# Optimization experiments

Measured on AMD Instinct MI355X. Metric: run time of the kernel, lower is better.

## Reference

```python
import jax, jax.numpy as jnp
import numpy as np

SINKHORN_ITERS = 100
SINKHORN_EPS = 0.1


def setup_inputs() -> dict:
    key = jax.random.key(0)
    k1, k2 = jax.random.split(key)
    M, N, C = 2048, 2048, 512
    d_M_q = jax.random.normal(k1, (M, C), dtype=jnp.float32)
    d_N_r = jax.random.normal(k2, (N, C), dtype=jnp.float32)
    # pipeline feeds L2-normalized descriptors (F.normalize(..., p=2, dim=1))
    d_M_q = d_M_q / jnp.linalg.norm(d_M_q, axis=1, keepdims=True)
    d_N_r = d_N_r / jnp.linalg.norm(d_N_r, axis=1, keepdims=True)
    z = jnp.float32(0.5)  # learned bin_score scalar
    return {"d_M_q": d_M_q, "d_N_r": d_N_r, "z": z}


def reference(d_M_q, d_N_r, z):
    M, N = d_M_q.shape[0], d_N_r.shape[0]
    # score matmul: (M, C) x (C, N) -> (M, N)
    score = jnp.einsum('mc,nc->mn', d_M_q, d_N_r)
    # augmented (M+1, N+1): dustbin row/col/corner filled with z
    S_aug = jnp.full((M + 1, N + 1), z, dtype=d_M_q.dtype).at[:M, :N].set(score)
    K0 = jnp.exp(S_aug / SINKHORN_EPS)

    def body(i, K):
        K = K / K.sum(axis=1, keepdims=True)  # row normalize
        K = K / K.sum(axis=0, keepdims=True)  # col normalize
        return K

    P_aug = jax.lax.fori_loop(0, SINKHORN_ITERS, body, K0)
    P = P_aug[:M, :N]
    return P, P_aug
```

## Files before the change

### kernel.cpp

```cpp
#include <hip/hip_runtime.h>
#include <hip/hip_fp16.h>

#define ITERS 100
#define AGENT __HIP_MEMORY_SCOPE_AGENT

union PK { unsigned long long u; struct { float v; unsigned tag; } s; };

#define SLOT 136
#define MSG_ONE (2 * 16 * 16 * SLOT)
#define UV_STRIDE 272

__device__ __forceinline__ float wave_sum(float p) {
    p += __shfl_xor(p, 1, 64);
    p += __shfl_xor(p, 2, 64);
    p += __shfl_xor(p, 4, 64);
    p += __shfl_xor(p, 8, 64);
    p += __shfl_xor(p, 16, 64);
    p += __shfl_xor(p, 32, 64);
    return p;
}

__global__ void __launch_bounds__(256, 1)
sinkhorn_fused(const float* __restrict__ Q, const float* __restrict__ R,
               const float* __restrict__ zp, float* __restrict__ out,
               unsigned long long* __restrict__ ws)
{
    __shared__ __align__(16) char smem[65536];
    float* As = (float*)smem;
    float* Bs = (float*)(smem + 32768);
    char*  TrmB = smem;
    char*  TcmB = smem + 32768;

    const int t  = threadIdx.x;
    const int b  = blockIdx.x;
    const int bi = b >> 4, bj = b & 15;
    const int tx = t & 15, ty = t >> 4;
    const int l  = t & 63, w  = t >> 6;
    const int gi0 = bi * 128, gj0 = bj * 128;

    float acc[8][8];
#pragma unroll
    for (int r = 0; r < 8; r++)
#pragma unroll
        for (int c = 0; c < 8; c++) acc[r][c] = 0.f;

    const int lr = t & 31, lc4 = t >> 5;
    const float* Qb = Q + (size_t)gi0 * 512;
    const float* Rb = R + (size_t)gj0 * 512;

    float4 qa[4], ra[4];
#pragma unroll
    for (int i = 0; i < 4; i++) {
        qa[i] = *(const float4*)(Qb + (size_t)(lr + 32 * i) * 512 + 4 * lc4);
        ra[i] = *(const float4*)(Rb + (size_t)(lr + 32 * i) * 512 + 4 * lc4);
    }
#pragma unroll
    for (int i = 0; i < 4; i++) {
        int row = lr + 32 * i;
        As[(4*lc4+0)*128 + row] = qa[i].x;  As[(4*lc4+1)*128 + row] = qa[i].y;
        As[(4*lc4+2)*128 + row] = qa[i].z;  As[(4*lc4+3)*128 + row] = qa[i].w;
        Bs[(4*lc4+0)*128 + row] = ra[i].x;  Bs[(4*lc4+1)*128 + row] = ra[i].y;
        Bs[(4*lc4+2)*128 + row] = ra[i].z;  Bs[(4*lc4+3)*128 + row] = ra[i].w;
    }
    __syncthreads();

    for (int ks = 0; ks < 16; ks++) {
        if (ks < 15) {
            int k0 = (ks + 1) * 32;
#pragma unroll
            for (int i = 0; i < 4; i++) {
                qa[i] = *(const float4*)(Qb + (size_t)(lr+32*i)*512 + k0 + 4*lc4);
                ra[i] = *(const float4*)(Rb + (size_t)(lr+32*i)*512 + k0 + 4*lc4);
            }
        }
        const float* A = As + (ks & 1) * (32 * 128);
        const float* B = Bs + (ks & 1) * (32 * 128);
#pragma unroll 4
        for (int k = 0; k < 32; k++) {
            float4 a0 = *(const float4*)(A + k*128 + 8*ty);
            float4 a1 = *(const float4*)(A + k*128 + 8*ty + 4);
            float4 b0 = *(const float4*)(B + k*128 + 8*tx);
            float4 b1 = *(const float4*)(B + k*128 + 8*tx + 4);
            float av[8] = {a0.x,a0.y,a0.z,a0.w,a1.x,a1.y,a1.z,a1.w};
            float bv[8] = {b0.x,b0.y,b0.z,b0.w,b1.x,b1.y,b1.z,b1.w};
#pragma unroll
            for (int r = 0; r < 8; r++)
#pragma unroll
                for (int c = 0; c < 8; c++)
                    acc[r][c] = fmaf(av[r], bv[c], acc[r][c]);
        }
        if (ks < 15) {
            __syncthreads();
            float* An = As + ((ks+1) & 1) * (32 * 128);
            float* Bn = Bs + ((ks+1) & 1) * (32 * 128);
#pragma unroll
            for (int i = 0; i < 4; i++) {
                int row = lr + 32 * i;
                An[(4*lc4+0)*128 + row] = qa[i].x;  An[(4*lc4+1)*128 + row] = qa[i].y;
                An[(4*lc4+2)*128 + row] = qa[i].z;  An[(4*lc4+3)*128 + row] = qa[i].w;
                Bn[(4*lc4+0)*128 + row] = ra[i].x;  Bn[(4*lc4+1)*128 + row] = ra[i].y;
                Bn[(4*lc4+2)*128 + row] = ra[i].z;  Bn[(4*lc4+3)*128 + row] = ra[i].w;
            }
            __syncthreads();
        }
    }
    __syncthreads();

    const float E = expf(zp[0] * 10.0f);
#pragma unroll
    for (int r = 0; r < 8; r++)
#pragma unroll
        for (int c = 0; c < 8; c++) acc[r][c] = expf(acc[r][c] * 10.0f);

#pragma unroll
    for (int r = 0; r < 8; r++) {
        int rr = 8 * ty + r;
        unsigned short h[8];
#pragma unroll
        for (int c = 0; c < 8; c++) h[c] = __half_as_ushort(__float2half(acc[r][c]));
        uint4 pk;
        pk.x = h[0] | ((unsigned)h[1] << 16); pk.y = h[2] | ((unsigned)h[3] << 16);
        pk.z = h[4] | ((unsigned)h[5] << 16); pk.w = h[6] | ((unsigned)h[7] << 16);
        *(uint4*)(TrmB + rr * 256 + ((tx ^ (rr & 15)) << 4)) = pk;
    }
#pragma unroll
    for (int c = 0; c < 8; c++) {
        int cc = 8 * tx + c;
        unsigned short h[8];
#pragma unroll
        for (int r = 0; r < 8; r++) h[r] = __half_as_ushort(__float2half(acc[r][c]));
        uint4 pk;
        pk.x = h[0] | ((unsigned)h[1] << 16); pk.y = h[2] | ((unsigned)h[3] << 16);
        pk.z = h[4] | ((unsigned)h[5] << 16); pk.w = h[6] | ((unsigned)h[7] << 16);
        *(uint4*)(TcmB + cc * 256 + ((ty ^ (cc & 15)) << 4)) = pk;
    }

    unsigned long long* rmsg = ws;
    unsigned long long* cmsg = ws + MSG_ONE;
    float* uvb  = (float*)(ws + 2 * MSG_ONE) + b * UV_STRIDE;
    float* ubuf = uvb;
    float* vbuf = uvb + 136;

    if (t < 128)      vbuf[t] = 1.0f;
    else if (t < 130) vbuf[t] = 64.0f;
    float uN = 0.f, vN = 1.0f, vsum = 128.0f, usum = 0.f;
    __syncthreads();

    for (int it = 0; it < ITERS; it++) {
        const int buf = it & 1;
        const unsigned tagw = (unsigned)(it + 1);

        {
            unsigned long long* base = rmsg + (size_t)((buf * 16 + bi) * 16) * SLOT;
            if (t == 128) {
                PK p; p.s.v = vsum; p.s.tag = tagw;
                __hip_atomic_store(base + (size_t)bj * SLOT + 128, p.u, __ATOMIC_RELAXED, AGENT);
            }
            if (t < 128) {
                const char* rp = TrmB + t * 256;
                const float4* v4 = (const float4*)vbuf;
                float racc = 0.f;
#pragma unroll
                for (int c = 0; c < 16; c++) {
                    uint4 kq = *(const uint4*)(rp + ((c ^ (t & 15)) << 4));
                    float4 va = v4[2 * c], vb = v4[2 * c + 1];
                    const __half2* h2 = (const __half2*)&kq;
                    float2 f;
                    f = __half22float2(h2[0]); racc = fmaf(f.x, va.x, fmaf(f.y, va.y, racc));
                    f = __half22float2(h2[1]); racc = fmaf(f.x, va.z, fmaf(f.y, va.w, racc));
                    f = __half22float2(h2[2]); racc = fmaf(f.x, vb.x, fmaf(f.y, vb.y, racc));
                    f = __half22float2(h2[3]); racc = fmaf(f.x, vb.z, fmaf(f.y, vb.w, racc));
                }
                PK p; p.s.v = racc; p.s.tag = tagw;
                __hip_atomic_store(base + (size_t)bj * SLOT + t, p.u, __ATOMIC_RELAXED, AGENT);
            }
            if (t < 128) {
                bool vdone = (l >= 16);
                float vsv = 0.f, rsum = 0.f;
                for (;;) {
                    PK m[16];
#pragma unroll
                    for (int s = 0; s < 16; s++)
                        m[s].u = __hip_atomic_load(base + (size_t)s * SLOT + t,
                                                   __ATOMIC_RELAXED, AGENT);
                    PK vm; vm.u = 0ull;
                    if (!vdone)
                        vm.u = __hip_atomic_load(base + (size_t)l * SLOT + 128,
                                                 __ATOMIC_RELAXED, AGENT);
                    int cnt = 0; float a = 0.f;
#pragma unroll
                    for (int s = 0; s < 16; s++) {
                        bool ok = (m[s].s.tag == tagw);
                        cnt += ok; a += ok ? m[s].s.v : 0.f;
                    }
                    if (!vdone && vm.s.tag == tagw) { vsv = vm.s.v; vdone = true; }
                    if (cnt == 16 && vdone) { rsum = a; break; }
                    __builtin_amdgcn_s_sleep(1);
                }
                float ssum = wave_sum(l < 16 ? vsv : 0.f);
                uN = 1.0f / (E * (ssum + vN));
                float ui = 1.0f / (rsum + E * vN);
                ubuf[t] = ui;
                float wsm = wave_sum(ui);
                if (l == 0) ubuf[128 + w] = wsm;
            }
            __syncthreads();
            usum = ubuf[128] + ubuf[129];
        }

        {
            unsigned long long* base = cmsg + (size_t)((buf * 16 + bj) * 16) * SLOT;
            if (t == 128) {
                PK p; p.s.v = usum; p.s.tag = tagw;
                __hip_atomic_store(base + (size_t)bi * SLOT + 128, p.u, __ATOMIC_RELAXED, AGENT);
            }
            if (t < 128) {
                const char* cp = TcmB + t * 256;
                const float4* u4 = (const float4*)ubuf;
                float cacc = 0.f;
#pragma unroll
                for (int c = 0; c < 16; c++) {
                    uint4 kq = *(const uint4*)(cp + ((c ^ (t & 15)) << 4));
                    float4 ua = u4[2 * c], ub = u4[2 * c + 1];
                    const __half2* h2 = (const __half2*)&kq;
                    float2 f;
                    f = __half22float2(h2[0]); cacc = fmaf(f.x, ua.x, fmaf(f.y, ua.y, cacc));
                    f = __half22float2(h2[1]); cacc = fmaf(f.x, ua.z, fmaf(f.y, ua.w, cacc));
                    f = __half22float2(h2[2]); cacc = fmaf(f.x, ub.x, fmaf(f.y, ub.y, cacc));
                    f = __half22float2(h2[3]); cacc = fmaf(f.x, ub.z, fmaf(f.y, ub.w, cacc));
                }
                PK p; p.s.v = cacc; p.s.tag = tagw;
                __hip_atomic_store(base + (size_t)bi * SLOT + t, p.u, __ATOMIC_RELAXED, AGENT);
            }
            if (t < 128) {
                bool udone = (l >= 16);
                float usv = 0.f, csum = 0.f;
                for (;;) {
                    PK m[16];
#pragma unroll
                    for (int s = 0; s < 16; s++)
                        m[s].u = __hip_atomic_load(base + (size_t)s * SLOT + t,
                                                   __ATOMIC_RELAXED, AGENT);
                    PK um; um.u = 0ull;
                    if (!udone)
                        um.u = __hip_atomic_load(base + (size_t)l * SLOT + 128,
                                                 __ATOMIC_RELAXED, AGENT);
                    int cnt = 0; float a = 0.f;
#pragma unroll
                    for (int s = 0; s < 16; s++) {
                        bool ok = (m[s].s.tag == tagw);
                        cnt += ok; a += ok ? m[s].s.v : 0.f;
                    }
                    if (!udone && um.s.tag == tagw) { usv = um.s.v; udone = true; }
                    if (cnt == 16 && udone) { csum = a; break; }
                    __builtin_amdgcn_s_sleep(1);
                }
                float ssum = wave_sum(l < 16 ? usv : 0.f);
                vN = 1.0f / (E * (ssum + uN));
                float vj = 1.0f / (csum + E * uN);
                vbuf[t] = vj;
                float wsm = wave_sum(vj);
                if (l == 0) vbuf[128 + w] = wsm;
            } else {
                bool udone = (l >= 16);
                float usv = 0.f;
                while (!udone) {
                    PK um;
                    um.u = __hip_atomic_load(base + (size_t)l * SLOT + 128,
                                             __ATOMIC_RELAXED, AGENT);
                    if (um.s.tag == tagw) { usv = um.s.v; udone = true; }
                    else __builtin_amdgcn_s_sleep(1);
                }
                float ssum = wave_sum(l < 16 ? usv : 0.f);
                vN = 1.0f / (E * (ssum + uN));
            }
            __syncthreads();
            vsum = vbuf[128] + vbuf[129];
        }
    }

    float* P  = out;
    float* PA = out + (size_t)2048 * 2048;
    float2 vv = *(const float2*)&vbuf[2 * l];
#pragma unroll 2
    for (int rr2 = 0; rr2 < 32; rr2++) {
        int i = 32 * w + rr2;
        float ui = ubuf[i];
        const char* rp = TrmB + i * 256;
        int c = l >> 2;
        __half2 h2 = *(const __half2*)(rp + ((c ^ (i & 15)) << 4) + (l & 3) * 4);
        float2 kf = __half22float2(h2);
        float p0 = ui * kf.x * vv.x;
        float p1 = ui * kf.y * vv.y;
        size_t gi = (size_t)(gi0 + i);
        *(float2*)&P[gi * 2048 + gj0 + 2 * l] = make_float2(p0, p1);
        PA[gi * 2049 + gj0 + 2 * l]     = p0;
        PA[gi * 2049 + gj0 + 2 * l + 1] = p1;
        if (bj == 15 && l == 0) PA[gi * 2049 + 2048] = ui * E * vN;
    }
    if (bi == 15 && w == 0) {
        PA[(size_t)2048 * 2049 + gj0 + 2 * l]     = uN * E * vv.x;
        PA[(size_t)2048 * 2049 + gj0 + 2 * l + 1] = uN * E * vv.y;
        if (bj == 15 && l == 0) PA[(size_t)2048 * 2049 + 2048] = uN * E * vN;
    }
}

extern "C" void kernel_launch(void* const* d_in, const int* in_sizes, int n_in,
                              void* d_out, int out_size, void* d_ws, size_t ws_size,
                              hipStream_t stream)
{
    (void)in_sizes; (void)n_in; (void)out_size; (void)ws_size;
    const float* Q  = (const float*)d_in[0];
    const float* R  = (const float*)d_in[1];
    const float* zp = (const float*)d_in[2];
    float* out = (float*)d_out;
    unsigned long long* ws = (unsigned long long*)d_ws;
    void* args[] = { (void*)&Q, (void*)&R, (void*)&zp, (void*)&out, (void*)&ws };
    hipLaunchCooperativeKernel((const void*)sinkhorn_fused, dim3(256), dim3(256),
                               args, 0, stream);
}
```

Before: 974.3 us.

## Split workgroup into row and column wave pairs with flag-based handoff

Replaces the per-iteration __syncthreads-driven sequence, in which waves 0-1 computed both row and column partials, with warp specialization. Waves 0-1 now own the row matvec and column wait, and waves 2-3 own the row-reduction wait and the column matvec. The two pairs hand off u/v vectors, partial sums and dustbin scalars through workgroup-scope global scratch flags and tags. The aim is to overlap waiting on cross-block messages with local compute and to drop block barriers. This adds spin-waits on global scratch and relies on manual memory ordering being correct.

```diff
diff --git a/kernel.cpp b/kernel.cpp
--- a/kernel.cpp
+++ b/kernel.cpp
@@ -3,12 +3,13 @@
 
 #define ITERS 100
 #define AGENT __HIP_MEMORY_SCOPE_AGENT
+#define WG    __HIP_MEMORY_SCOPE_WORKGROUP
 
 union PK { unsigned long long u; struct { float v; unsigned tag; } s; };
 
 #define SLOT 136
 #define MSG_ONE (2 * 16 * 16 * SLOT)
-#define UV_STRIDE 272
+#define SCRF 320
 
 __device__ __forceinline__ float wave_sum(float p) {
     p += __shfl_xor(p, 1, 64);
@@ -137,29 +138,37 @@
 
     unsigned long long* rmsg = ws;
     unsigned long long* cmsg = ws + MSG_ONE;
-    float* uvb  = (float*)(ws + 2 * MSG_ONE) + b * UV_STRIDE;
-    float* ubuf = uvb;
-    float* vbuf = uvb + 136;
-
-    if (t < 128)      vbuf[t] = 1.0f;
-    else if (t < 130) vbuf[t] = 64.0f;
-    float uN = 0.f, vN = 1.0f, vsum = 128.0f, usum = 0.f;
+    float* fb   = (float*)(ws + 2 * MSG_ONE) + (size_t)b * SCRF;
+    float* ubuf = fb;
+    float* vbuf = fb + 128;
+    float* psum = fb + 256;
+    unsigned* flg = (unsigned*)(fb + 260);
+    unsigned long long* uNm = (unsigned long long*)(fb + 264);
+    unsigned long long* vNm = (unsigned long long*)(fb + 266);
+
+    if (t < 128) vbuf[t] = 1.0f;
+    if (t == 0) {
+        flg[0] = 0; flg[1] = 0; flg[2] = 0; flg[3] = 0;
+        PK p0; p0.s.v = 0.0f; p0.s.tag = 0u; *uNm = p0.u;
+        PK p1; p1.s.v = 1.0f; p1.s.tag = 0u; *vNm = p1.u;
+    }
     __syncthreads();
 
-    for (int it = 0; it < ITERS; it++) {
-        const int buf = it & 1;
-        const unsigned tagw = (unsigned)(it + 1);
-
-        {
-            unsigned long long* base = rmsg + (size_t)((buf * 16 + bi) * 16) * SLOT;
-            if (t == 128) {
+    if (t < 128) {
+        float vsum = 128.0f;
+        for (int it = 0; it < ITERS; ++it) {
+            const int buf = it & 1;
+            const unsigned tagw = (unsigned)(it + 1);
+            unsigned long long* ub = rmsg + (size_t)((buf * 16 + bi) * 16) * SLOT;
+
+            if (t == 0) {
                 PK p; p.s.v = vsum; p.s.tag = tagw;
-                __hip_atomic_store(base + (size_t)bj * SLOT + 128, p.u, __ATOMIC_RELAXED, AGENT);
-            }
-            if (t < 128) {
+                __hip_atomic_store(ub + (size_t)bj * SLOT + 128, p.u, __ATOMIC_RELAXED, AGENT);
+            }
+            float racc = 0.f;
+            {
                 const char* rp = TrmB + t * 256;
                 const float4* v4 = (const float4*)vbuf;
-                float racc = 0.f;
 #pragma unroll
                 for (int c = 0; c < 16; c++) {
                     uint4 kq = *(const uint4*)(rp + ((c ^ (t & 15)) << 4));
@@ -171,113 +180,132 @@
                     f = __half22float2(h2[2]); racc = fmaf(f.x, vb.x, fmaf(f.y, vb.y, racc));
                     f = __half22float2(h2[3]); racc = fmaf(f.x, vb.z, fmaf(f.y, vb.w, racc));
                 }
-                PK p; p.s.v = racc; p.s.tag = tagw;
-                __hip_atomic_store(base + (size_t)bj * SLOT + t, p.u, __ATOMIC_RELAXED, AGENT);
-            }
-            if (t < 128) {
-                bool vdone = (l >= 16);
-                float vsv = 0.f, rsum = 0.f;
-                for (;;) {
-                    PK m[16];
-#pragma unroll
-                    for (int s = 0; s < 16; s++)
-                        m[s].u = __hip_atomic_load(base + (size_t)s * SLOT + t,
-                                                   __ATOMIC_RELAXED, AGENT);
-                    PK vm; vm.u = 0ull;
-                    if (!vdone)
-                        vm.u = __hip_atomic_load(base + (size_t)l * SLOT + 128,
-                                                 __ATOMIC_RELAXED, AGENT);
-                    int cnt = 0; float a = 0.f;
-#pragma unroll
-                    for (int s = 0; s < 16; s++) {
-                        bool ok = (m[s].s.tag == tagw);
-                        cnt += ok; a += ok ? m[s].s.v : 0.f;
-                    }
-                    if (!vdone && vm.s.tag == tagw) { vsv = vm.s.v; vdone = true; }
-                    if (cnt == 16 && vdone) { rsum = a; break; }
-                    __builtin_amdgcn_s_sleep(1);
+            }
+            { PK p; p.s.v = racc; p.s.tag = tagw;
+              __hip_atomic_store(ub + (size_t)bj * SLOT + t, p.u, __ATOMIC_RELAXED, AGENT); }
+
+            unsigned long long* cb = cmsg + (size_t)((buf * 16 + bj) * 16) * SLOT;
+            bool udone = (l >= 16);
+            float usv = 0.f, csum = 0.f;
+            for (;;) {
+                PK m[16];
+#pragma unroll
+                for (int s = 0; s < 16; s++)
+                    m[s].u = __hip_atomic_load(cb + (size_t)s * SLOT + t,
+                                               __ATOMIC_RELAXED, AGENT);
+                PK um; um.u = 0ull;
+                if (!udone)
+                    um.u = __hip_atomic_load(cb + (size_t)l * SLOT + 128,
+                                             __ATOMIC_RELAXED, AGENT);
+                int cnt = 0; float a = 0.f;
+#pragma unroll
+                for (int s = 0; s < 16; s++) {
+                    bool ok = (m[s].s.tag == tagw);
+                    cnt += ok; a += ok ? m[s].s.v : 0.f;
                 }
-                float ssum = wave_sum(l < 16 ? vsv : 0.f);
-                uN = 1.0f / (E * (ssum + vN));
-                float ui = 1.0f / (rsum + E * vN);
-                ubuf[t] = ui;
-                float wsm = wave_sum(ui);
-                if (l == 0) ubuf[128 + w] = wsm;
-            }
-            __syncthreads();
-            usum = ubuf[128] + ubuf[129];
-        }
-
-        {
-            unsigned long long* base = cmsg + (size_t)((buf * 16 + bj) * 16) * SLOT;
-            if (t == 128) {
-                PK p; p.s.v = usum; p.s.tag = tagw;
-                __hip_atomic_store(base + (size_t)bi * SLOT + 128, p.u, __ATOMIC_RELAXED, AGENT);
-            }
-            if (t < 128) {
-                const char* cp = TcmB + t * 256;
+                if (!udone && um.s.tag == tagw) { usv = um.s.v; udone = true; }
+                if (cnt == 16 && udone) { csum = a; break; }
+                __builtin_amdgcn_s_sleep(1);
+            }
+            float ssum = wave_sum(l < 16 ? usv : 0.f);
+            PK un;
+            for (;;) {
+                un.u = __hip_atomic_load(uNm, __ATOMIC_RELAXED, WG);
+                if (un.s.tag == tagw) break;
+                __builtin_amdgcn_s_sleep(1);
+            }
+            const float uNv = un.s.v;
+            const float vNv = 1.0f / (E * (ssum + uNv));
+            float vj = 1.0f / (csum + E * uNv);
+            vbuf[t] = vj;
+            float wsm = wave_sum(vj);
+            if (l == 0) psum[2 + w] = wsm;
+            if (t == 0) { PK p; p.s.v = vNv; p.s.tag = tagw;
+                          __hip_atomic_store(vNm, p.u, __ATOMIC_RELAXED, WG); }
+            asm volatile("s_waitcnt vmcnt(0)" ::: "memory");
+            if (l == 0) __hip_atomic_store(&flg[2 + w], tagw, __ATOMIC_RELEASE, WG);
+            while (__hip_atomic_load(&flg[2 + (w ^ 1)], __ATOMIC_ACQUIRE, WG) < tagw)
+                __builtin_amdgcn_s_sleep(1);
+            vsum = psum[2] + psum[3];
+        }
+    } else {
+        const int tr = t - 128;
+        const int pw = w - 2;
+        for (int it = 0; it < ITERS; ++it) {
+            const int buf = it & 1;
+            const unsigned tagw = (unsigned)(it + 1);
+            unsigned long long* ub = rmsg + (size_t)((buf * 16 + bi) * 16) * SLOT;
+
+            bool vdone = (l >= 16);
+            float vsv = 0.f, rsum = 0.f;
+            for (;;) {
+                PK m[16];
+#pragma unroll
+                for (int s = 0; s < 16; s++)
+                    m[s].u = __hip_atomic_load(ub + (size_t)s * SLOT + tr,
+                                               __ATOMIC_RELAXED, AGENT);
+                PK vm; vm.u = 0ull;
+                if (!vdone)
+                    vm.u = __hip_atomic_load(ub + (size_t)l * SLOT + 128,
+                                             __ATOMIC_RELAXED, AGENT);
+                int cnt = 0; float a = 0.f;
+#pragma unroll
+                for (int s = 0; s < 16; s++) {
+                    bool ok = (m[s].s.tag == tagw);
+                    cnt += ok; a += ok ? m[s].s.v : 0.f;
+                }
+                if (!vdone && vm.s.tag == tagw) { vsv = vm.s.v; vdone = true; }
+                if (cnt == 16 && vdone) { rsum = a; break; }
+                __builtin_amdgcn_s_sleep(1);
+            }
+            float ssum = wave_sum(l < 16 ? vsv : 0.f);
+            PK vn;
+            for (;;) {
+                vn.u = __hip_atomic_load(vNm, __ATOMIC_RELAXED, WG);
+                if (vn.s.tag == (unsigned)it) break;
+                __builtin_amdgcn_s_sleep(1);
+            }
+            const float vNv = vn.s.v;
+            const float uNv = 1.0f / (E * (ssum + vNv));
+            float ui = 1.0f / (rsum + E * vNv);
+            ubuf[tr] = ui;
+            float wsm = wave_sum(ui);
+            if (l == 0) psum[pw] = wsm;
+            if (t == 128) { PK p; p.s.v = uNv; p.s.tag = tagw;
+                            __hip_atomic_store(uNm, p.u, __ATOMIC_RELAXED, WG); }
+            asm volatile("s_waitcnt vmcnt(0)" ::: "memory");
+            if (l == 0) __hip_atomic_store(&flg[pw], tagw, __ATOMIC_RELEASE, WG);
+            while (__hip_atomic_load(&flg[pw ^ 1], __ATOMIC_ACQUIRE, WG) < tagw)
+                __builtin_amdgcn_s_sleep(1);
+            float usum = psum[0] + psum[1];
+
+            unsigned long long* cb = cmsg + (size_t)((buf * 16 + bj) * 16) * SLOT;
+            if (t == 128) { PK p; p.s.v = usum; p.s.tag = tagw;
+                __hip_atomic_store(cb + (size_t)bi * SLOT + 128, p.u, __ATOMIC_RELAXED, AGENT); }
+            float cacc = 0.f;
+            {
+                const char* cp = TcmB + tr * 256;
                 const float4* u4 = (const float4*)ubuf;
-                float cacc = 0.f;
 #pragma unroll
                 for (int c = 0; c < 16; c++) {
-                    uint4 kq = *(const uint4*)(cp + ((c ^ (t & 15)) << 4));
-                    float4 ua = u4[2 * c], ub = u4[2 * c + 1];
+                    uint4 kq = *(const uint4*)(cp + ((c ^ (tr & 15)) << 4));
+                    float4 ua = u4[2 * c], ub2 = u4[2 * c + 1];
                     const __half2* h2 = (const __half2*)&kq;
                     float2 f;
                     f = __half22float2(h2[0]); cacc = fmaf(f.x, ua.x, fmaf(f.y, ua.y, cacc));
                     f = __half22float2(h2[1]); cacc = fmaf(f.x, ua.z, fmaf(f.y, ua.w, cacc));
-                    f = __half22float2(h2[2]); cacc = fmaf(f.x, ub.x, fmaf(f.y, ub.y, cacc));
-                    f = __half22float2(h2[3]); cacc = fmaf(f.x, ub.z, fmaf(f.y, ub.w, cacc));
+                    f = __half22float2(h2[2]); cacc = fmaf(f.x, ub2.x, fmaf(f.y, ub2.y, cacc));
+                    f = __half22float2(h2[3]); cacc = fmaf(f.x, ub2.z, fmaf(f.y, ub2.w, cacc));
                 }
-                PK p; p.s.v = cacc; p.s.tag = tagw;
-                __hip_atomic_store(base + (size_t)bi * SLOT + t, p.u, __ATOMIC_RELAXED, AGENT);
-            }
-            if (t < 128) {
-                bool udone = (l >= 16);
-                float usv = 0.f, csum = 0.f;
-                for (;;) {
-                    PK m[16];
-#pragma unroll
-                    for (int s = 0; s < 16; s++)
-                        m[s].u = __hip_atomic_load(base + (size_t)s * SLOT + t,
-                                                   __ATOMIC_RELAXED, AGENT);
-                    PK um; um.u = 0ull;
-                    if (!udone)
-                        um.u = __hip_atomic_load(base + (size_t)l * SLOT + 128,
-                                                 __ATOMIC_RELAXED, AGENT);
-                    int cnt = 0; float a = 0.f;
-#pragma unroll
-                    for (int s = 0; s < 16; s++) {
-                        bool ok = (m[s].s.tag == tagw);
-                        cnt += ok; a += ok ? m[s].s.v : 0.f;
-                    }
-                    if (!udone && um.s.tag == tagw) { usv = um.s.v; udone = true; }
-                    if (cnt == 16 && udone) { csum = a; break; }
-                    __builtin_amdgcn_s_sleep(1);
-                }
-                float ssum = wave_sum(l < 16 ? usv : 0.f);
-                vN = 1.0f / (E * (ssum + uN));
-                float vj = 1.0f / (csum + E * uN);
-                vbuf[t] = vj;
-                float wsm = wave_sum(vj);
-                if (l == 0) vbuf[128 + w] = wsm;
-            } else {
-                bool udone = (l >= 16);
-                float usv = 0.f;
-                while (!udone) {
-                    PK um;
-                    um.u = __hip_atomic_load(base + (size_t)l * SLOT + 128,
-                                             __ATOMIC_RELAXED, AGENT);
-                    if (um.s.tag == tagw) { usv = um.s.v; udone = true; }
-                    else __builtin_amdgcn_s_sleep(1);
-                }
-                float ssum = wave_sum(l < 16 ? usv : 0.f);
-                vN = 1.0f / (E * (ssum + uN));
-            }
-            __syncthreads();
-            vsum = vbuf[128] + vbuf[129];
-        }
-    }
+            }
+            { PK p; p.s.v = cacc; p.s.tag = tagw;
+              __hip_atomic_store(cb + (size_t)bi * SLOT + tr, p.u, __ATOMIC_RELAXED, AGENT); }
+        }
+    }
+    __syncthreads();
+
+    PK uNp, vNp; uNp.u = *uNm; vNp.u = *vNm;
+    const float uN = uNp.s.v, vN = vNp.s.v;
 
     float* P  = out;
     float* PA = out + (size_t)2048 * 2048;
```

Result: slower. 1.292 ms (+32.6%).

## Replace tagged message slots with biased double atomic-add accumulators

Applied to the files above, without the earlier changes.

Each iteration's cross-block row and column sums were exchanged by writing tagged slots that 16 consumers then polled one by one. Blocks now atomically add their partial sums into per-iteration double cells, each carrying a +2^32 bias, and poll a single cell until all 16 bias contributions have arrived. The dustbin totals are published by the diagonal blocks only, and u/v buffers move into shared memory. This cuts each thread's polling from 16 loads to one, at the cost of atomic contention, a larger per-iteration workspace and an extra memset before launch.

```diff
diff --git a/kernel.cpp b/kernel.cpp
--- a/kernel.cpp
+++ b/kernel.cpp
@@ -4,11 +4,11 @@
 #define ITERS 100
 #define AGENT __HIP_MEMORY_SCOPE_AGENT
 
-union PK { unsigned long long u; struct { float v; unsigned tag; } s; };
-
-#define SLOT 136
-#define MSG_ONE (2 * 16 * 16 * SLOT)
-#define UV_STRIDE 272
+#define UACC_OFF 0
+#define VACC_OFF ((size_t)ITERS * 2048 * 2)
+#define UTOT_OFF (2 * VACC_OFF)
+#define VTOT_OFF (UTOT_OFF + (size_t)ITERS * 16 * 2)
+#define WS_F64   (VTOT_OFF + (size_t)ITERS * 16 * 2)
 
 __device__ __forceinline__ float wave_sum(float p) {
     p += __shfl_xor(p, 1, 64);
@@ -20,16 +20,35 @@
     return p;
 }
 
+__device__ __forceinline__ void acc_add(double* cell, float val) {
+    __hip_atomic_fetch_add(cell, (double)val + 4294967296.0,
+                           __ATOMIC_RELAXED, AGENT);
+}
+__device__ __forceinline__ float poll16(const double* cell) {
+    const unsigned long long* p = (const unsigned long long*)cell;
+    for (;;) {
+        unsigned long long x = __hip_atomic_load(p, __ATOMIC_RELAXED, AGENT);
+        if (x >= 0x4230000000000000ull)
+            return (float)(__longlong_as_double(x) - 68719476736.0);
+        __builtin_amdgcn_s_sleep(1);
+    }
+}
+
 __global__ void __launch_bounds__(256, 1)
 sinkhorn_fused(const float* __restrict__ Q, const float* __restrict__ R,
                const float* __restrict__ zp, float* __restrict__ out,
-               unsigned long long* __restrict__ ws)
+               double* __restrict__ acc)
 {
-    __shared__ __align__(16) char smem[65536];
+    __shared__ __align__(16) char smem[66624];
     float* As = (float*)smem;
     float* Bs = (float*)(smem + 32768);
     char*  TrmB = smem;
     char*  TcmB = smem + 32768;
+    float* ubuf = (float*)(smem + 65536);
+    float* vbuf = (float*)(smem + 66048);
+    float* redU = (float*)(smem + 66560);
+    float* redV = (float*)(smem + 66568);
+    float* sc   = (float*)(smem + 66576);
 
     const int t  = threadIdx.x;
     const int b  = blockIdx.x;
@@ -38,11 +57,11 @@
     const int l  = t & 63, w  = t >> 6;
     const int gi0 = bi * 128, gj0 = bj * 128;
 
-    float acc[8][8];
+    float a8[8][8];
 #pragma unroll
     for (int r = 0; r < 8; r++)
 #pragma unroll
-        for (int c = 0; c < 8; c++) acc[r][c] = 0.f;
+        for (int c = 0; c < 8; c++) a8[r][c] = 0.f;
 
     const int lr = t & 31, lc4 = t >> 5;
     const float* Qb = Q + (size_t)gi0 * 512;
@@ -87,7 +106,7 @@
             for (int r = 0; r < 8; r++)
 #pragma unroll
                 for (int c = 0; c < 8; c++)
-                    acc[r][c] = fmaf(av[r], bv[c], acc[r][c]);
+                    a8[r][c] = fmaf(av[r], bv[c], a8[r][c]);
         }
         if (ks < 15) {
             __syncthreads();
@@ -110,14 +129,14 @@
 #pragma unroll
     for (int r = 0; r < 8; r++)
 #pragma unroll
-        for (int c = 0; c < 8; c++) acc[r][c] = expf(acc[r][c] * 10.0f);
+        for (int c = 0; c < 8; c++) a8[r][c] = expf(a8[r][c] * 10.0f);
 
 #pragma unroll
     for (int r = 0; r < 8; r++) {
         int rr = 8 * ty + r;
         unsigned short h[8];
 #pragma unroll
-        for (int c = 0; c < 8; c++) h[c] = __half_as_ushort(__float2half(acc[r][c]));
+        for (int c = 0; c < 8; c++) h[c] = __half_as_ushort(__float2half(a8[r][c]));
         uint4 pk;
         pk.x = h[0] | ((unsigned)h[1] << 16); pk.y = h[2] | ((unsigned)h[3] << 16);
         pk.z = h[4] | ((unsigned)h[5] << 16); pk.w = h[6] | ((unsigned)h[7] << 16);
@@ -128,34 +147,25 @@
         int cc = 8 * tx + c;
         unsigned short h[8];
 #pragma unroll
-        for (int r = 0; r < 8; r++) h[r] = __half_as_ushort(__float2half(acc[r][c]));
+        for (int r = 0; r < 8; r++) h[r] = __half_as_ushort(__float2half(a8[r][c]));
         uint4 pk;
         pk.x = h[0] | ((unsigned)h[1] << 16); pk.y = h[2] | ((unsigned)h[3] << 16);
         pk.z = h[4] | ((unsigned)h[5] << 16); pk.w = h[6] | ((unsigned)h[7] << 16);
         *(uint4*)(TcmB + cc * 256 + ((ty ^ (cc & 15)) << 4)) = pk;
     }
 
-    unsigned long long* rmsg = ws;
-    unsigned long long* cmsg = ws + MSG_ONE;
-    float* uvb  = (float*)(ws + 2 * MSG_ONE) + b * UV_STRIDE;
-    float* ubuf = uvb;
-    float* vbuf = uvb + 136;
-
-    if (t < 128)      vbuf[t] = 1.0f;
-    else if (t < 130) vbuf[t] = 64.0f;
-    float uN = 0.f, vN = 1.0f, vsum = 128.0f, usum = 0.f;
+    double* uacc = acc + UACC_OFF;
+    double* vacc = acc + VACC_OFF;
+    double* utot = acc + UTOT_OFF;
+    double* vtot = acc + VTOT_OFF;
+    const bool diag = (bi == bj);
+
+    if (t < 128) vbuf[t] = 1.0f;
+    float uN = 0.f, vN = 1.0f;
     __syncthreads();
 
     for (int it = 0; it < ITERS; it++) {
-        const int buf = it & 1;
-        const unsigned tagw = (unsigned)(it + 1);
-
         {
-            unsigned long long* base = rmsg + (size_t)((buf * 16 + bi) * 16) * SLOT;
-            if (t == 128) {
-                PK p; p.s.v = vsum; p.s.tag = tagw;
-                __hip_atomic_store(base + (size_t)bj * SLOT + 128, p.u, __ATOMIC_RELAXED, AGENT);
-            }
             if (t < 128) {
                 const char* rp = TrmB + t * 256;
                 const float4* v4 = (const float4*)vbuf;
@@ -171,49 +181,31 @@
                     f = __half22float2(h2[2]); racc = fmaf(f.x, vb.x, fmaf(f.y, vb.y, racc));
                     f = __half22float2(h2[3]); racc = fmaf(f.x, vb.z, fmaf(f.y, vb.w, racc));
                 }
-                PK p; p.s.v = racc; p.s.tag = tagw;
-                __hip_atomic_store(base + (size_t)bj * SLOT + t, p.u, __ATOMIC_RELAXED, AGENT);
-            }
-            if (t < 128) {
-                bool vdone = (l >= 16);
-                float vsv = 0.f, rsum = 0.f;
-                for (;;) {
-                    PK m[16];
-#pragma unroll
-                    for (int s = 0; s < 16; s++)
-                        m[s].u = __hip_atomic_load(base + (size_t)s * SLOT + t,
-                                                   __ATOMIC_RELAXED, AGENT);
-                    PK vm; vm.u = 0ull;
-                    if (!vdone)
-                        vm.u = __hip_atomic_load(base + (size_t)l * SLOT + 128,
-                                                 __ATOMIC_RELAXED, AGENT);
-                    int cnt = 0; float a = 0.f;
-#pragma unroll
-                    for (int s = 0; s < 16; s++) {
-                        bool ok = (m[s].s.tag == tagw);
-                        cnt += ok; a += ok ? m[s].s.v : 0.f;
-                    }
-                    if (!vdone && vm.s.tag == tagw) { vsv = vm.s.v; vdone = true; }
-                    if (cnt == 16 && vdone) { rsum = a; break; }
-                    __builtin_amdgcn_s_sleep(1);
-                }
-                float ssum = wave_sum(l < 16 ? vsv : 0.f);
-                uN = 1.0f / (E * (ssum + vN));
+                acc_add(uacc + ((size_t)it * 2048 + 128 * bi + t) * 2, racc);
+            } else if (t == 128) {
+                sc[0] = (it == 0) ? 2048.0f
+                                  : poll16(vtot + ((size_t)it * 16 + bi) * 2);
+            }
+            if (t < 128) {
+                float rsum = poll16(uacc + ((size_t)it * 2048 + 128 * bi + t) * 2);
                 float ui = 1.0f / (rsum + E * vN);
                 ubuf[t] = ui;
                 float wsm = wave_sum(ui);
-                if (l == 0) ubuf[128 + w] = wsm;
-            }
-            __syncthreads();
-            usum = ubuf[128] + ubuf[129];
+                if (l == 0) redU[w] = wsm;
+            }
+            __syncthreads();
+            uN = 1.0f / (E * (sc[0] + vN));
+            if (diag && t == 128) {
+                float usum = redU[0] + redU[1];
+                double* ub = utot + (size_t)it * 16 * 2;
+#pragma unroll
+                for (int g = 0; g < 16; g++)
+                    __hip_atomic_fetch_add(ub + g * 2, (double)usum + 4294967296.0,
+                                           __ATOMIC_RELAXED, AGENT);
+            }
         }
 
         {
-            unsigned long long* base = cmsg + (size_t)((buf * 16 + bj) * 16) * SLOT;
-            if (t == 128) {
-                PK p; p.s.v = usum; p.s.tag = tagw;
-                __hip_atomic_store(base + (size_t)bi * SLOT + 128, p.u, __ATOMIC_RELAXED, AGENT);
-            }
             if (t < 128) {
                 const char* cp = TcmB + t * 256;
                 const float4* u4 = (const float4*)ubuf;
@@ -229,53 +221,27 @@
                     f = __half22float2(h2[2]); cacc = fmaf(f.x, ub.x, fmaf(f.y, ub.y, cacc));
                     f = __half22float2(h2[3]); cacc = fmaf(f.x, ub.z, fmaf(f.y, ub.w, cacc));
                 }
-                PK p; p.s.v = cacc; p.s.tag = tagw;
-                __hip_atomic_store(base + (size_t)bi * SLOT + t, p.u, __ATOMIC_RELAXED, AGENT);
-            }
-            if (t < 128) {
-                bool udone = (l >= 16);
-                float usv = 0.f, csum = 0.f;
-                for (;;) {
-                    PK m[16];
-#pragma unroll
-                    for (int s = 0; s < 16; s++)
-                        m[s].u = __hip_atomic_load(base + (size_t)s * SLOT + t,
-                                                   __ATOMIC_RELAXED, AGENT);
-                    PK um; um.u = 0ull;
-                    if (!udone)
-                        um.u = __hip_atomic_load(base + (size_t)l * SLOT + 128,
-                                                 __ATOMIC_RELAXED, AGENT);
-                    int cnt = 0; float a = 0.f;
-#pragma unroll
-                    for (int s = 0; s < 16; s++) {
-                        bool ok = (m[s].s.tag == tagw);
-                        cnt += ok; a += ok ? m[s].s.v : 0.f;
-                    }
-                    if (!udone && um.s.tag == tagw) { usv = um.s.v; udone = true; }
-                    if (cnt == 16 && udone) { csum = a; break; }
-                    __builtin_amdgcn_s_sleep(1);
-                }
-                float ssum = wave_sum(l < 16 ? usv : 0.f);
-                vN = 1.0f / (E * (ssum + uN));
+                acc_add(vacc + ((size_t)it * 2048 + 128 * bj + t) * 2, cacc);
+            } else if (t == 128) {
+                sc[1] = poll16(utot + ((size_t)it * 16 + bi) * 2);
+            }
+            if (t < 128) {
+                float csum = poll16(vacc + ((size_t)it * 2048 + 128 * bj + t) * 2);
                 float vj = 1.0f / (csum + E * uN);
                 vbuf[t] = vj;
                 float wsm = wave_sum(vj);
-                if (l == 0) vbuf[128 + w] = wsm;
-            } else {
-                bool udone = (l >= 16);
-                float usv = 0.f;
-                while (!udone) {
-                    PK um;
-                    um.u = __hip_atomic_load(base + (size_t)l * SLOT + 128,
-                                             __ATOMIC_RELAXED, AGENT);
-                    if (um.s.tag == tagw) { usv = um.s.v; udone = true; }
-                    else __builtin_amdgcn_s_sleep(1);
-                }
-                float ssum = wave_sum(l < 16 ? usv : 0.f);
-                vN = 1.0f / (E * (ssum + uN));
-            }
-            __syncthreads();
-            vsum = vbuf[128] + vbuf[129];
+                if (l == 0) redV[w] = wsm;
+            }
+            __syncthreads();
+            vN = 1.0f / (E * (sc[1] + uN));
+            if (diag && t == 128 && it + 1 < ITERS) {
+                float vsum = redV[0] + redV[1];
+                double* vb = vtot + (size_t)(it + 1) * 16 * 2;
+#pragma unroll
+                for (int g = 0; g < 16; g++)
+                    __hip_atomic_fetch_add(vb + g * 2, (double)vsum + 4294967296.0,
+                                           __ATOMIC_RELAXED, AGENT);
+            }
         }
     }
 
@@ -314,8 +280,9 @@
     const float* R  = (const float*)d_in[1];
     const float* zp = (const float*)d_in[2];
     float* out = (float*)d_out;
-    unsigned long long* ws = (unsigned long long*)d_ws;
-    void* args[] = { (void*)&Q, (void*)&R, (void*)&zp, (void*)&out, (void*)&ws };
+    double* acc = (double*)d_ws;
+    hipMemsetAsync(d_ws, 0, WS_F64 * sizeof(double), stream);
+    void* args[] = { (void*)&Q, (void*)&R, (void*)&zp, (void*)&out, (void*)&acc };
     hipLaunchCooperativeKernel((const void*)sinkhorn_fused, dim3(256), dim3(256),
                                args, 0, stream);
 }
```

Result: slower. 1.517 ms (+55.7%).
